# Kernel tuning notes

Measured on AMD Instinct MI355X. Metric: run time of the kernel, lower is better.

## Reference

```python
import jax, jax.numpy as jnp
import numpy as np
from itertools import permutations

EPS = 1e-14


def setup_inputs() -> dict:
    key = jax.random.key(0)
    k1, k2 = jax.random.split(key)
    B, T, S = 512, 8000, 3
    pred = jax.random.normal(k1, (B, T, S), dtype=jnp.float32)
    targets = (jax.random.uniform(k2, (B, T, S)) < 0.3).astype(jnp.float32)
    mask = jnp.ones((B, T), dtype=jnp.float32)
    return {"pred_frames_out": pred, "targets": targets, "mask": mask}


def _pit_loss(pred, targets, mask):
    # pred, targets: [B, T, S]; mask: [B, T]
    B, T, S = pred.shape
    x = pred[:, :, :, None]        # [B,T,S_pred,1]
    t = targets[:, :, None, :]     # [B,T,1,S_tgt]
    # numerically stable BCE-with-logits (same as nn.BCEWithLogitsLoss)
    bce = jnp.maximum(x, 0.0) - x * t + jnp.log1p(jnp.exp(-jnp.abs(x)))  # [B,T,S,S]
    msum = jnp.sum(mask, axis=1) + EPS                                    # [B]
    # cost[b,i,j] = masked mean over time of BCE(pred_i, target_j)
    cost = jnp.einsum('btij,bt->bij', bce, mask) / msum[:, None, None]    # [B,S,S]
    perms = jnp.asarray(list(permutations(range(S))), dtype=jnp.int32)    # [P,S]
    idx_i = jnp.arange(S)[None, :]                                        # [1,S]
    # perm_loss[b,p] = mean_i cost[b, i, perms[p,i]]
    perm_loss = jnp.mean(cost[:, idx_i, perms], axis=-1)                  # [B,P]
    best_val = jnp.min(perm_loss, axis=1)                                 # [B]
    best_idx = jnp.argmin(perm_loss, axis=1)                              # [B]
    return best_val.mean(), best_idx


def reference(pred_frames_out, targets, mask):
    return _pit_loss(pred_frames_out, targets, mask)
```

## Files before the change

### kernel.cpp

```cpp
#include <hip/hip_runtime.h>
#include <math.h>

#define BB 512
#define TT 8000
#define SS 3
#define CH 4
#define TC (TT/CH)
#define NV (TC/4)
#define NACC 13
#define NWAVE 4
#define WPB (BB*CH*NWAVE)

__device__ __forceinline__ double waveReduceD(double v) {
    #pragma unroll
    for (int o = 32; o > 0; o >>= 1) v += __shfl_down(v, o, 64);
    return v;
}

__device__ __forceinline__ void accum_elem(float acc[NACC], float m,
                                           float x0, float x1, float x2,
                                           float t0, float t1, float t2) {
    acc[12] += m;
    float x[3] = {x0, x1, x2};
    float t[3] = {t0, t1, t2};
    #pragma unroll
    for (int i = 0; i < 3; i++) {
        float xi = x[i];
        float sp = fmaxf(xi, 0.0f) + __logf(1.0f + __expf(-fabsf(xi)));
        acc[i] = fmaf(m, sp, acc[i]);
        float mx = m * xi;
        #pragma unroll
        for (int j = 0; j < 3; j++)
            acc[3 + i*3 + j] = fmaf(mx, t[j], acc[3 + i*3 + j]);
    }
}

__device__ __forceinline__ void accum_item(float acc[NACC],
                                           float4 pa, float4 pb, float4 pc,
                                           float4 ta, float4 tb, float4 tc,
                                           float4 mm) {
    accum_elem(acc, mm.x, pa.x, pa.y, pa.z, ta.x, ta.y, ta.z);
    accum_elem(acc, mm.y, pa.w, pb.x, pb.y, ta.w, tb.x, tb.y);
    accum_elem(acc, mm.z, pb.z, pb.w, pc.x, tb.z, tb.w, tc.x);
    accum_elem(acc, mm.w, pc.y, pc.z, pc.w, tc.y, tc.z, tc.w);
}

__global__ __launch_bounds__(256) void pit_partial(
        const float* __restrict__ pred,
        const float* __restrict__ tgt,
        const float* __restrict__ mask,
        float* __restrict__ wpart) {
    int blk = blockIdx.x;
    int b = blk >> 2, c = blk & 3;
    int tbase = c * TC;
    const float* pp = pred + ((size_t)b * TT + tbase) * 3;
    const float* tp = tgt  + ((size_t)b * TT + tbase) * 3;
    const float* mp = mask + (size_t)b * TT + tbase;

    int tid = threadIdx.x;
    int i0 = tid;
    int i1 = tid + 256;
    bool v1 = (i1 < NV);
    int i1c = v1 ? i1 : (NV - 1);

    const float4* p40 = (const float4*)(pp + (size_t)i0 * 12);
    const float4* t40 = (const float4*)(tp + (size_t)i0 * 12);
    float4 pa0 = p40[0], pb0 = p40[1], pc0 = p40[2];
    float4 ta0 = t40[0], tb0 = t40[1], tc0 = t40[2];
    float4 mm0 = *(const float4*)(mp + (size_t)i0 * 4);

    const float4* p41 = (const float4*)(pp + (size_t)i1c * 12);
    const float4* t41 = (const float4*)(tp + (size_t)i1c * 12);
    float4 pa1 = p41[0], pb1 = p41[1], pc1 = p41[2];
    float4 ta1 = t41[0], tb1 = t41[1], tc1 = t41[2];
    float4 mm1 = *(const float4*)(mp + (size_t)i1c * 4);
    if (!v1) { mm1.x = mm1.y = mm1.z = mm1.w = 0.0f; }

    float acc[NACC];
    #pragma unroll
    for (int k = 0; k < NACC; k++) acc[k] = 0.0f;

    accum_item(acc, pa0, pb0, pc0, ta0, tb0, tc0, mm0);
    accum_item(acc, pa1, pb1, pc1, ta1, tb1, tc1, mm1);

    #pragma unroll
    for (int k = 0; k < NACC; k++) {
        float v = acc[k];
        #pragma unroll
        for (int o = 32; o > 0; o >>= 1) v += __shfl_xor(v, o, 64);
        acc[k] = v;
    }

    int lane = tid & 63, wave = tid >> 6;
    if (lane == 0) {
        float* dst = wpart + ((size_t)blk * NWAVE + wave) * NACC;
        #pragma unroll
        for (int k = 0; k < NACC; k++) dst[k] = acc[k];
    }
}

__global__ __launch_bounds__(64) void pit_finalize(
        const float* __restrict__ wpart,
        double* __restrict__ bestv,
        float* __restrict__ out) {
    int b = blockIdx.x * 64 + threadIdx.x;
    if (b >= BB) return;
    const float* p = wpart + (size_t)b * (CH * NWAVE * NACC);
    double acc[NACC];
    #pragma unroll
    for (int k = 0; k < NACC; k++) acc[k] = 0.0;
    #pragma unroll
    for (int g = 0; g < CH * NWAVE; g++)
        #pragma unroll
        for (int k = 0; k < NACC; k++)
            acc[k] += (double)p[g * NACC + k];

    double msum = acc[12] + 1e-14;
    double cost[3][3];
    #pragma unroll
    for (int i = 0; i < 3; i++)
        #pragma unroll
        for (int j = 0; j < 3; j++)
            cost[i][j] = (acc[i] - acc[3 + i*3 + j]) / msum;

    const int perms[6][3] = {{0,1,2},{0,2,1},{1,0,2},{1,2,0},{2,0,1},{2,1,0}};
    double best = 1e300; int bidx = 0;
    #pragma unroll
    for (int p6 = 0; p6 < 6; p6++) {
        double v = (cost[0][perms[p6][0]] + cost[1][perms[p6][1]] +
                    cost[2][perms[p6][2]]) / 3.0;
        if (v < best) { best = v; bidx = p6; }
    }
    bestv[b] = best;
    out[1 + b] = (float)bidx;
}

__global__ __launch_bounds__(256) void pit_mean(
        const double* __restrict__ bestv, float* __restrict__ out) {
    __shared__ double sd[4];
    double v = 0.0;
    for (int b = threadIdx.x; b < BB; b += 256) v += bestv[b];
    int lane = threadIdx.x & 63, wave = threadIdx.x >> 6;
    v = waveReduceD(v);
    if (lane == 0) sd[wave] = v;
    __syncthreads();
    if (threadIdx.x == 0) {
        double s = sd[0] + sd[1] + sd[2] + sd[3];
        out[0] = (float)(s / (double)BB);
    }
}

extern "C" void kernel_launch(void* const* d_in, const int* in_sizes, int n_in,
                              void* d_out, int out_size, void* d_ws, size_t ws_size,
                              hipStream_t stream) {
    const float* pred = (const float*)d_in[0];
    const float* tgt  = (const float*)d_in[1];
    const float* mask = (const float*)d_in[2];
    float* out = (float*)d_out;

    float* wpart  = (float*)d_ws;
    double* bestv = (double*)((char*)d_ws + ((WPB * NACC * 4 + 255) & ~255));

    pit_partial<<<BB * CH, 256, 0, stream>>>(pred, tgt, mask, wpart);
    pit_finalize<<<(BB + 63) / 64, 64, 0, stream>>>(wpart, bestv, out);
    pit_mean<<<1, 256, 0, stream>>>(bestv, out);
}
```

Baseline: 32.25 us.

## Fuse partial and finalize into per-batch block with double-buffered global_load_lds pipeline

Replaces the 4-chunk-per-batch partial kernel and separate finalize kernel with one block per batch. Each wave streams seven 1024-frame tiles through LDS using direct global-to-LDS loads, double-buffered with vmcnt waits. A register-loaded tail covers the last frames, and the 3x3 cost and permutation search run in-block. This drops one launch and the workspace round trip, at the cost of only 512 blocks and more serial work per block, which may reduce memory-level parallelism.

```diff
diff --git a/kernel.cpp b/kernel.cpp
--- a/kernel.cpp
+++ b/kernel.cpp
@@ -3,19 +3,26 @@
 
 #define BB 512
 #define TT 8000
-#define SS 3
-#define CH 4
-#define TC (TT/CH)
-#define NV (TC/4)
+#define TILE 1024
+#define NTILE 7
+#define TAILB (NTILE*TILE)
+#define TAILN (TT-TAILB)
+#define TAILIT (TAILN/4)
 #define NACC 13
-#define NWAVE 4
-#define WPB (BB*CH*NWAVE)
 
-__device__ __forceinline__ double waveReduceD(double v) {
-    #pragma unroll
-    for (int o = 32; o > 0; o >>= 1) v += __shfl_down(v, o, 64);
-    return v;
+#define BUF_F 1792
+#define SLICE_F (2*BUF_F)
+
+__device__ __forceinline__ void ld16(const float4* g, float* l) {
+    __builtin_amdgcn_global_load_lds(
+        (const __attribute__((address_space(1))) void*)g,
+        (__attribute__((address_space(3))) void*)l, 16, 0, 0);
 }
+
+#define WAIT_VM7() { asm volatile("s_waitcnt vmcnt(7)" ::: "memory"); \
+                     __builtin_amdgcn_sched_barrier(0); }
+#define WAIT_VM0() { asm volatile("s_waitcnt vmcnt(0)" ::: "memory"); \
+                     __builtin_amdgcn_sched_barrier(0); }
 
 __device__ __forceinline__ void accum_elem(float acc[NACC], float m,
                                            float x0, float x1, float x2,
@@ -45,43 +52,74 @@
     accum_elem(acc, mm.w, pc.y, pc.z, pc.w, tc.y, tc.z, tc.w);
 }
 
-__global__ __launch_bounds__(256) void pit_partial(
+__global__ __launch_bounds__(256) void pit_batch(
         const float* __restrict__ pred,
         const float* __restrict__ tgt,
         const float* __restrict__ mask,
-        float* __restrict__ wpart) {
-    int blk = blockIdx.x;
-    int b = blk >> 2, c = blk & 3;
-    int tbase = c * TC;
-    const float* pp = pred + ((size_t)b * TT + tbase) * 3;
-    const float* tp = tgt  + ((size_t)b * TT + tbase) * 3;
-    const float* mp = mask + (size_t)b * TT + tbase;
+        double* __restrict__ bestv,
+        float* __restrict__ out) {
+    __shared__ float lds[4 * SLICE_F];
+    __shared__ float red[4][NACC];
 
-    int tid = threadIdx.x;
-    int i0 = tid;
-    int i1 = tid + 256;
-    bool v1 = (i1 < NV);
-    int i1c = v1 ? i1 : (NV - 1);
+    int b = blockIdx.x;
+    int tid = threadIdx.x, lane = tid & 63, w = tid >> 6;
+    const float* pb = pred + (size_t)b * TT * 3;
+    const float* tb = tgt  + (size_t)b * TT * 3;
+    const float* mb = mask + (size_t)b * TT;
 
-    const float4* p40 = (const float4*)(pp + (size_t)i0 * 12);
-    const float4* t40 = (const float4*)(tp + (size_t)i0 * 12);
-    float4 pa0 = p40[0], pb0 = p40[1], pc0 = p40[2];
-    float4 ta0 = t40[0], tb0 = t40[1], tc0 = t40[2];
-    float4 mm0 = *(const float4*)(mp + (size_t)i0 * 4);
+    int it = tid < TAILIT ? tid : (TAILIT - 1);
+    const float4* tp = (const float4*)(pb + (size_t)(TAILB + 4*it) * 3);
+    const float4* tt = (const float4*)(tb + (size_t)(TAILB + 4*it) * 3);
+    float4 PA = tp[0], PB = tp[1], PC = tp[2];
+    float4 TA = tt[0], TB = tt[1], TC = tt[2];
+    float4 MM = *(const float4*)(mb + TAILB + 4*it);
 
-    const float4* p41 = (const float4*)(pp + (size_t)i1c * 12);
-    const float4* t41 = (const float4*)(tp + (size_t)i1c * 12);
-    float4 pa1 = p41[0], pb1 = p41[1], pc1 = p41[2];
-    float4 ta1 = t41[0], tb1 = t41[1], tc1 = t41[2];
-    float4 mm1 = *(const float4*)(mp + (size_t)i1c * 4);
-    if (!v1) { mm1.x = mm1.y = mm1.z = mm1.w = 0.0f; }
+    float* slice = lds + w * SLICE_F;
+    const float4* pg4 = (const float4*)pb;
+    const float4* tg4 = (const float4*)tb;
+    const float4* mg4 = (const float4*)mb;
+
+    #define STAGE(u, d) { \
+        float* base_ = slice + (d) * BUF_F; \
+        const float4* p_ = pg4 + (size_t)(u)*768 + w*192 + lane; \
+        const float4* t_ = tg4 + (size_t)(u)*768 + w*192 + lane; \
+        const float4* m_ = mg4 + (size_t)(u)*256 + w*64  + lane; \
+        ld16(p_,       base_); \
+        ld16(p_ + 64,  base_ + 256); \
+        ld16(p_ + 128, base_ + 512); \
+        ld16(t_,       base_ + 768); \
+        ld16(t_ + 64,  base_ + 1024); \
+        ld16(t_ + 128, base_ + 1280); \
+        ld16(m_,       base_ + 1536); \
+    }
 
     float acc[NACC];
     #pragma unroll
     for (int k = 0; k < NACC; k++) acc[k] = 0.0f;
 
-    accum_item(acc, pa0, pb0, pc0, ta0, tb0, tc0, mm0);
-    accum_item(acc, pa1, pb1, pc1, ta1, tb1, tc1, mm1);
+    STAGE(0, 0);
+
+    #pragma unroll
+    for (int u = 0; u < NTILE; u++) {
+        if (u + 1 < NTILE) {
+            STAGE(u + 1, (u + 1) & 1);
+            WAIT_VM7();
+        } else {
+            WAIT_VM0();
+        }
+        const float* base = slice + (u & 1) * BUF_F;
+        #pragma unroll
+        for (int u2 = 0; u2 < 4; u2++) {
+            int e = lane + 64 * u2;
+            float m = base[1536 + e];
+            accum_elem(acc, m, base[3*e], base[3*e+1], base[3*e+2],
+                       base[768 + 3*e], base[768 + 3*e+1], base[768 + 3*e+2]);
+        }
+        __builtin_amdgcn_sched_barrier(0);
+    }
+
+    if (tid >= TAILIT) { MM.x = MM.y = MM.z = MM.w = 0.0f; }
+    accum_item(acc, PA, PB, PC, TA, TB, TC, MM);
 
     #pragma unroll
     for (int k = 0; k < NACC; k++) {
@@ -90,58 +128,46 @@
         for (int o = 32; o > 0; o >>= 1) v += __shfl_xor(v, o, 64);
         acc[k] = v;
     }
-
-    int lane = tid & 63, wave = tid >> 6;
     if (lane == 0) {
-        float* dst = wpart + ((size_t)blk * NWAVE + wave) * NACC;
         #pragma unroll
-        for (int k = 0; k < NACC; k++) dst[k] = acc[k];
+        for (int k = 0; k < NACC; k++) red[w][k] = acc[k];
     }
-}
-
-__global__ __launch_bounds__(64) void pit_finalize(
-        const float* __restrict__ wpart,
-        double* __restrict__ bestv,
-        float* __restrict__ out) {
-    int b = blockIdx.x * 64 + threadIdx.x;
-    if (b >= BB) return;
-    const float* p = wpart + (size_t)b * (CH * NWAVE * NACC);
-    double acc[NACC];
-    #pragma unroll
-    for (int k = 0; k < NACC; k++) acc[k] = 0.0;
-    #pragma unroll
-    for (int g = 0; g < CH * NWAVE; g++)
+    __syncthreads();
+    if (tid == 0) {
+        double a[NACC];
         #pragma unroll
         for (int k = 0; k < NACC; k++)
-            acc[k] += (double)p[g * NACC + k];
-
-    double msum = acc[12] + 1e-14;
-    double cost[3][3];
-    #pragma unroll
-    for (int i = 0; i < 3; i++)
+            a[k] = (double)red[0][k] + (double)red[1][k] +
+                   (double)red[2][k] + (double)red[3][k];
+        double msum = a[12] + 1e-14;
+        double cost[3][3];
         #pragma unroll
-        for (int j = 0; j < 3; j++)
-            cost[i][j] = (acc[i] - acc[3 + i*3 + j]) / msum;
-
-    const int perms[6][3] = {{0,1,2},{0,2,1},{1,0,2},{1,2,0},{2,0,1},{2,1,0}};
-    double best = 1e300; int bidx = 0;
-    #pragma unroll
-    for (int p6 = 0; p6 < 6; p6++) {
-        double v = (cost[0][perms[p6][0]] + cost[1][perms[p6][1]] +
-                    cost[2][perms[p6][2]]) / 3.0;
-        if (v < best) { best = v; bidx = p6; }
+        for (int i = 0; i < 3; i++)
+            #pragma unroll
+            for (int j = 0; j < 3; j++)
+                cost[i][j] = (a[i] - a[3 + i*3 + j]) / msum;
+        const int perms[6][3] = {{0,1,2},{0,2,1},{1,0,2},
+                                 {1,2,0},{2,0,1},{2,1,0}};
+        double best = 1e300; int bidx = 0;
+        #pragma unroll
+        for (int p = 0; p < 6; p++) {
+            double v = (cost[0][perms[p][0]] + cost[1][perms[p][1]] +
+                        cost[2][perms[p][2]]) / 3.0;
+            if (v < best) { best = v; bidx = p; }
+        }
+        bestv[b] = best;
+        out[1 + b] = (float)bidx;
     }
-    bestv[b] = best;
-    out[1 + b] = (float)bidx;
 }
 
 __global__ __launch_bounds__(256) void pit_mean(
         const double* __restrict__ bestv, float* __restrict__ out) {
     __shared__ double sd[4];
     double v = 0.0;
-    for (int b = threadIdx.x; b < BB; b += 256) v += bestv[b];
+    for (int i = threadIdx.x; i < BB; i += 256) v += bestv[i];
     int lane = threadIdx.x & 63, wave = threadIdx.x >> 6;
-    v = waveReduceD(v);
+    #pragma unroll
+    for (int o = 32; o > 0; o >>= 1) v += __shfl_down(v, o, 64);
     if (lane == 0) sd[wave] = v;
     __syncthreads();
     if (threadIdx.x == 0) {
@@ -157,11 +183,8 @@
     const float* tgt  = (const float*)d_in[1];
     const float* mask = (const float*)d_in[2];
     float* out = (float*)d_out;
+    double* bestv = (double*)d_ws;
 
-    float* wpart  = (float*)d_ws;
-    double* bestv = (double*)((char*)d_ws + ((WPB * NACC * 4 + 255) & ~255));
-
-    pit_partial<<<BB * CH, 256, 0, stream>>>(pred, tgt, mask, wpart);
-    pit_finalize<<<(BB + 63) / 64, 64, 0, stream>>>(wpart, bestv, out);
+    pit_batch<<<BB, 256, 0, stream>>>(pred, tgt, mask, bestv, out);
     pit_mean<<<1, 256, 0, stream>>>(bestv, out);
 }
```

Result: no change. 32.21 us (-0.1%).
